# Performance work log

Measured on AMD Instinct MI355X. Metric: run time of the kernel, lower is better.

Reference implementation:

```python
import jax, jax.numpy as jnp
import numpy as np
from jax import lax

N, C_IN, H, W = 32, 128, 64, 64
C_OUT, KH, KW = 256, 3, 3
C_DIM = 64


def setup_inputs() -> dict:
    key = jax.random.key(0)
    k1, k2, k3, k4, k5 = jax.random.split(key, 5)
    return {
        "x": jax.random.normal(k1, (N, C_IN, H, W), dtype=jnp.float32),
        "c": jax.random.normal(k2, (N, C_DIM), dtype=jnp.float32),
        "weight": jax.random.normal(k3, (C_OUT, C_IN, KH, KW), dtype=jnp.float32),
        "c_weight": jax.random.normal(k4, (C_OUT, C_DIM), dtype=jnp.float32),
        "bias": jax.random.normal(k5, (C_OUT,), dtype=jnp.float32),
    }


def reference(x, c, weight, c_weight, bias):
    # Equivalent to the module's unfold + matmul path (groups=1, dilation=1,
    # zero padding=1, stride=1): a direct conv fused with the spatially
    # invariant context bias c @ c_weight^T and the channel bias.
    out = lax.conv_general_dilated(
        x, weight,
        window_strides=(1, 1),
        padding=((1, 1), (1, 1)),
        dimension_numbers=("NCHW", "OIHW", "NCHW"),
    )  # (N, C_out, H, W)
    ctx = jnp.einsum("nd,od->no", c, c_weight)  # (N, C_out), same at every spatial loc
    return out + ctx[:, :, None, None] + bias[None, :, None, None]
```

## Files before the change

kernel.cpp:

```cpp
#include <hip/hip_runtime.h>
#include <hip/hip_bf16.h>


#define NN   32
#define CIN  128
#define HH   64
#define WW   64
#define COUT 256
#define CDIM 64
#define HP   66
#define WP   66

#define XP_BYTES  ((size_t)NN*HP*WP*CIN*2)
#define WT_BYTES  ((size_t)9*COUT*CIN*2)
#define CTX_BYTES ((size_t)NN*COUT*4)
#define WS_NEEDED (XP_BYTES + WT_BYTES + CTX_BYTES)

typedef __attribute__((ext_vector_type(8))) short short8;
typedef __attribute__((ext_vector_type(4))) float float4v;

__device__ __forceinline__ void async16(const void* g, void* l) {
    __builtin_amdgcn_global_load_lds(
        (const __attribute__((address_space(1))) unsigned int*)g,
        (__attribute__((address_space(3))) unsigned int*)l, 16, 0, 0);
}

__global__ __launch_bounds__(256) void zero_halo(__hip_bfloat16* __restrict__ xP) {
    int g = blockIdx.x * 256 + threadIdx.x;
    int n   = g / 4160;
    int rem = g - n * 4160;
    int pi  = rem >> 4;
    int oct = rem & 15;
    int hh, ww;
    if (pi < 132) { hh = (pi >= 66) ? 65 : 0; ww = pi % 66; }
    else { int p2 = pi - 132; ww = (p2 >= 64) ? 65 : 0; hh = 1 + (p2 & 63); }
    short8 z = {};
    *(short8*)(xP + (((size_t)n * HP + hh) * WP + ww) * CIN + oct * 8) = z;
}

__global__ __launch_bounds__(256) void prep_x(const float* __restrict__ x,
                                              __hip_bfloat16* __restrict__ xP) {
    __shared__ float tile[CIN][65];
    int n = blockIdx.x >> 6;
    int h = blockIdx.x & 63;
    int t = threadIdx.x;
    const float* xb = x + (size_t)n * CIN * HH * WW + (size_t)h * WW;

    int lane16 = t & 15, rgrp = t >> 4;
    #pragma unroll
    for (int i = 0; i < 8; ++i) {
        int ci = rgrp + i * 16;
        float4v v = *(const float4v*)(xb + (size_t)ci * (HH * WW) + lane16 * 4);
        int w0 = lane16 * 4;
        tile[ci][w0]     = v.x;
        tile[ci][w0 + 1] = v.y;
        tile[ci][w0 + 2] = v.z;
        tile[ci][w0 + 3] = v.w;
    }
    __syncthreads();

    int oct = t & 3, w = t >> 2;
    __hip_bfloat16* db = xP + (((size_t)n * HP + (h + 1)) * WP + (w + 1)) * CIN;
    #pragma unroll
    for (int p = 0; p < 4; ++p) {
        int ci0 = p * 32 + oct * 8;
        union { short8 v; __hip_bfloat16 b[8]; } u;
        #pragma unroll
        for (int j = 0; j < 8; ++j)
            u.b[j] = __float2bfloat16(tile[ci0 + j][w]);
        *(short8*)(db + ci0) = u.v;
    }
}

__global__ __launch_bounds__(256) void prep_wc(const float* __restrict__ wgt,
                                               const float* __restrict__ c,
                                               const float* __restrict__ cw,
                                               const float* __restrict__ bias,
                                               __hip_bfloat16* __restrict__ wT,
                                               float* __restrict__ ctx) {
    int bid = blockIdx.x;
    if (bid < 1152) {
        int idx = bid * 256 + threadIdx.x;
        int ci  = idx & 127;
        int co  = (idx >> 7) & 255;
        int tap = idx >> 15;
        wT[idx] = __float2bfloat16(wgt[((size_t)co * CIN + ci) * 9 + tap]);
    } else {
        int idx = (bid - 1152) * 256 + threadIdx.x;
        int co = idx & 255, n = idx >> 8;
        float a = bias[co];
        #pragma unroll 8
        for (int d = 0; d < CDIM; ++d) a += c[n * CDIM + d] * cw[co * CDIM + d];
        ctx[idx] = a;
    }
}

__global__ __launch_bounds__(256) void conv_mfma(
    const __hip_bfloat16* __restrict__ xP,
    const __hip_bfloat16* __restrict__ wT,
    const float* __restrict__ ctx,
    float* __restrict__ out)
{
    __shared__ __align__(16) short A_s[8192];
    __shared__ __align__(16) short B_s[8192];

    int bid = blockIdx.x;
    int nt  = bid & 1;
    int mt  = bid >> 1;
    int n   = mt >> 5;
    int h0  = (mt & 31) << 1;

    int tid = threadIdx.x;
    int lane = tid & 63, wv = tid >> 6;
    int m0 = (wv & 1) * 64, n0 = (wv >> 1) * 64;

    int p0   = wv * 8 + (lane >> 3);
    int q8   = ((lane & 7) ^ (lane >> 3)) * 8;
    int dst0 = wv * 512 + lane * 8;

    int cofs0 = ((0 * 4 + (lane >> 4)) ^ (lane & 7)) * 8;
    int cofs1 = ((1 * 4 + (lane >> 4)) ^ (lane & 7)) * 8;

    float4v acc[4][4] = {};

    for (int kh = 0; kh < 3; ++kh)
    for (int kw = 0; kw < 3; ++kw) {
        int tap = kh * 3 + kw;
        #pragma unroll
        for (int kb = 0; kb < 2; ++kb) {
            __syncthreads();
            #pragma unroll
            for (int i = 0; i < 4; ++i) {
                int p  = p0 + i * 32;
                int hh = h0 + (p >> 6) + kh;
                int ww = (p & 63) + kw;
                const __hip_bfloat16* asrc =
                    xP + (((size_t)n * HP + hh) * WP + ww) * CIN + kb * 64 + q8;
                async16(asrc, &A_s[i * 2048 + dst0]);
                const __hip_bfloat16* bsrc =
                    wT + ((size_t)tap * COUT + nt * 128 + p) * CIN + kb * 64 + q8;
                async16(bsrc, &B_s[i * 2048 + dst0]);
            }
            __syncthreads();

            #pragma unroll
            for (int kk = 0; kk < 2; ++kk) {
                int cofs = kk ? cofs1 : cofs0;
                short8 aF[4], bF[4];
                #pragma unroll
                for (int mi = 0; mi < 4; ++mi)
                    aF[mi] = *(const short8*)&A_s[(m0 + mi * 16 + (lane & 15)) * 64 + cofs];
                #pragma unroll
                for (int ni = 0; ni < 4; ++ni)
                    bF[ni] = *(const short8*)&B_s[(n0 + ni * 16 + (lane & 15)) * 64 + cofs];
                #pragma unroll
                for (int mi = 0; mi < 4; ++mi)
                    #pragma unroll
                    for (int ni = 0; ni < 4; ++ni)
                        acc[mi][ni] = __builtin_amdgcn_mfma_f32_16x16x32_bf16(
                            aF[mi], bF[ni], acc[mi][ni], 0, 0, 0);
            }
        }
    }

    #pragma unroll
    for (int ni = 0; ni < 4; ++ni) {
        int co = nt * 128 + n0 + ni * 16 + (lane & 15);
        float cv = ctx[n * COUT + co];
        #pragma unroll
        for (int mi = 0; mi < 4; ++mi) {
            int rp = m0 + mi * 16 + (lane >> 4) * 4;
            int hh = h0 + (rp >> 6);
            int ww = rp & 63;
            float4v v = acc[mi][ni] + cv;
            *(float4v*)&out[(((size_t)n * COUT + co) * HH + hh) * WW + ww] = v;
        }
    }
}

__global__ __launch_bounds__(256) void contextual_conv_f32(
    const float* __restrict__ x, const float* __restrict__ c,
    const float* __restrict__ wgt, const float* __restrict__ cw,
    const float* __restrict__ bias, float* __restrict__ out)
{
    int idx = blockIdx.x * 256 + threadIdx.x;
    int w = idx & 63, h = (idx >> 6) & 63, cb = (idx >> 12) & 63, n = idx >> 18;
    float acc[4];
    #pragma unroll
    for (int j = 0; j < 4; ++j) acc[j] = bias[cb + j * 64];
    const float* cp = c + n * CDIM;
    for (int d = 0; d < CDIM; ++d) {
        float cv = cp[d];
        #pragma unroll
        for (int j = 0; j < 4; ++j) acc[j] += cv * cw[(cb + j * 64) * CDIM + d];
    }
    const float* xn = x + (size_t)n * (CIN * HH * WW);
    for (int ci = 0; ci < CIN; ++ci) {
        const float* xc = xn + ci * (HH * WW);
        float wv[4][9];
        #pragma unroll
        for (int j = 0; j < 4; ++j) {
            const float* wp = wgt + ((cb + j * 64) * CIN + ci) * 9;
            #pragma unroll
            for (int k = 0; k < 9; ++k) wv[j][k] = wp[k];
        }
        #pragma unroll
        for (int kh = 0; kh < 3; ++kh) {
            int hh = h + kh - 1;
            if (hh < 0 || hh >= HH) continue;
            const float* xr = xc + hh * WW;
            #pragma unroll
            for (int kw = 0; kw < 3; ++kw) {
                int ww = w + kw - 1;
                if (ww < 0 || ww >= WW) continue;
                float xv = xr[ww];
                #pragma unroll
                for (int j = 0; j < 4; ++j) acc[j] += xv * wv[j][kh * 3 + kw];
            }
        }
    }
    size_t obase = (size_t)n * (COUT * HH * WW) + (size_t)h * WW + w;
    #pragma unroll
    for (int j = 0; j < 4; ++j)
        out[obase + (size_t)(cb + j * 64) * (HH * WW)] = acc[j];
}

extern "C" void kernel_launch(void* const* d_in, const int* in_sizes, int n_in,
                              void* d_out, int out_size, void* d_ws, size_t ws_size,
                              hipStream_t stream) {
    const float* x    = (const float*)d_in[0];
    const float* c    = (const float*)d_in[1];
    const float* wgt  = (const float*)d_in[2];
    const float* cw   = (const float*)d_in[3];
    const float* bias = (const float*)d_in[4];
    float* out = (float*)d_out;

    if (ws_size < WS_NEEDED) {
        const int total_threads = NN * 64 * HH * WW;
        contextual_conv_f32<<<total_threads / 256, 256, 0, stream>>>(x, c, wgt, cw, bias, out);
        return;
    }

    char* ws = (char*)d_ws;
    __hip_bfloat16* xP = (__hip_bfloat16*)ws;
    __hip_bfloat16* wT = (__hip_bfloat16*)(ws + XP_BYTES);
    float*          cx = (float*)(ws + XP_BYTES + WT_BYTES);

    zero_halo<<<520, 256, 0, stream>>>(xP);
    prep_x  <<<NN * HH, 256, 0, stream>>>(x, xP);
    prep_wc <<<1184, 256, 0, stream>>>(wgt, c, cw, bias, wT, cx);
    conv_mfma<<<2048, 256, 0, stream>>>(xP, wT, cx, out);
}
```

Measured before the change: 270.5 us.

## Merge prep kernels and enlarge conv tile with double-buffered LDS pipeline

Folds the halo-zeroing, input-transpose and weight/context prep kernels into one launch, cutting launch overhead. The conv kernel now uses 512-thread blocks computing 256 output pixels by all 256 output channels. That halves the weight reloads per pixel and doubles per-wave accumulator tiles (8x4). LDS is double-buffered so the next tap's async global-to-LDS loads overlap the current MFMA work, with one barrier per step. Block indices are swizzled across images. The costs are higher register and LDS use (128 KB), which lowers occupancy, and a grid of only 512 blocks.

```diff
diff --git a/kernel.cpp b/kernel.cpp
--- a/kernel.cpp
+++ b/kernel.cpp
@@ -25,155 +25,168 @@
         (__attribute__((address_space(3))) unsigned int*)l, 16, 0, 0);
 }
 
-__global__ __launch_bounds__(256) void zero_halo(__hip_bfloat16* __restrict__ xP) {
-    int g = blockIdx.x * 256 + threadIdx.x;
-    int n   = g / 4160;
-    int rem = g - n * 4160;
-    int pi  = rem >> 4;
-    int oct = rem & 15;
-    int hh, ww;
-    if (pi < 132) { hh = (pi >= 66) ? 65 : 0; ww = pi % 66; }
-    else { int p2 = pi - 132; ww = (p2 >= 64) ? 65 : 0; hh = 1 + (p2 & 63); }
-    short8 z = {};
-    *(short8*)(xP + (((size_t)n * HP + hh) * WP + ww) * CIN + oct * 8) = z;
-}
-
-__global__ __launch_bounds__(256) void prep_x(const float* __restrict__ x,
-                                              __hip_bfloat16* __restrict__ xP) {
+__global__ __launch_bounds__(256) void prep_all(
+    const float* __restrict__ x, const float* __restrict__ c,
+    const float* __restrict__ wgt, const float* __restrict__ cw,
+    const float* __restrict__ bias,
+    __hip_bfloat16* __restrict__ xP, __hip_bfloat16* __restrict__ wT,
+    float* __restrict__ ctx)
+{
     __shared__ float tile[CIN][65];
-    int n = blockIdx.x >> 6;
-    int h = blockIdx.x & 63;
-    int t = threadIdx.x;
-    const float* xb = x + (size_t)n * CIN * HH * WW + (size_t)h * WW;
-
-    int lane16 = t & 15, rgrp = t >> 4;
-    #pragma unroll
-    for (int i = 0; i < 8; ++i) {
-        int ci = rgrp + i * 16;
-        float4v v = *(const float4v*)(xb + (size_t)ci * (HH * WW) + lane16 * 4);
-        int w0 = lane16 * 4;
-        tile[ci][w0]     = v.x;
-        tile[ci][w0 + 1] = v.y;
-        tile[ci][w0 + 2] = v.z;
-        tile[ci][w0 + 3] = v.w;
-    }
-    __syncthreads();
-
-    int oct = t & 3, w = t >> 2;
-    __hip_bfloat16* db = xP + (((size_t)n * HP + (h + 1)) * WP + (w + 1)) * CIN;
-    #pragma unroll
-    for (int p = 0; p < 4; ++p) {
-        int ci0 = p * 32 + oct * 8;
-        union { short8 v; __hip_bfloat16 b[8]; } u;
-        #pragma unroll
-        for (int j = 0; j < 8; ++j)
-            u.b[j] = __float2bfloat16(tile[ci0 + j][w]);
-        *(short8*)(db + ci0) = u.v;
-    }
-}
-
-__global__ __launch_bounds__(256) void prep_wc(const float* __restrict__ wgt,
-                                               const float* __restrict__ c,
-                                               const float* __restrict__ cw,
-                                               const float* __restrict__ bias,
-                                               __hip_bfloat16* __restrict__ wT,
-                                               float* __restrict__ ctx) {
     int bid = blockIdx.x;
-    if (bid < 1152) {
-        int idx = bid * 256 + threadIdx.x;
-        int ci  = idx & 127;
-        int co  = (idx >> 7) & 255;
-        int tap = idx >> 15;
-        wT[idx] = __float2bfloat16(wgt[((size_t)co * CIN + ci) * 9 + tap]);
+    int t   = threadIdx.x;
+
+    if (bid < 2048) {
+        int n = bid >> 6;
+        int h = bid & 63;
+        const float* xb = x + (size_t)n * CIN * HH * WW + (size_t)h * WW;
+
+        int lane16 = t & 15, rgrp = t >> 4;
+        #pragma unroll
+        for (int i = 0; i < 8; ++i) {
+            int ci = rgrp + i * 16;
+            float4v v = *(const float4v*)(xb + (size_t)ci * (HH * WW) + lane16 * 4);
+            int w0 = lane16 * 4;
+            tile[ci][w0]     = v.x;
+            tile[ci][w0 + 1] = v.y;
+            tile[ci][w0 + 2] = v.z;
+            tile[ci][w0 + 3] = v.w;
+        }
+        __syncthreads();
+
+        int oct = t & 3, w = t >> 2;
+        __hip_bfloat16* db = xP + (((size_t)n * HP + (h + 1)) * WP + (w + 1)) * CIN;
+        #pragma unroll
+        for (int p = 0; p < 4; ++p) {
+            int ci0 = p * 32 + oct * 8;
+            union { short8 v; __hip_bfloat16 b[8]; } u;
+            #pragma unroll
+            for (int j = 0; j < 8; ++j)
+                u.b[j] = __float2bfloat16(tile[ci0 + j][w]);
+            *(short8*)(db + ci0) = u.v;
+        }
+    } else if (bid < 2568) {
+        int g = (bid - 2048) * 256 + t;
+        int n   = g / 4160;
+        int rem = g - n * 4160;
+        int pi  = rem >> 4;
+        int oct = rem & 15;
+        int hh, ww;
+        if (pi < 132) { hh = (pi >= 66) ? 65 : 0; ww = pi % 66; }
+        else { int p2 = pi - 132; ww = (p2 >= 64) ? 65 : 0; hh = 1 + (p2 & 63); }
+        short8 z = {};
+        *(short8*)(xP + (((size_t)n * HP + hh) * WP + ww) * CIN + oct * 8) = z;
     } else {
-        int idx = (bid - 1152) * 256 + threadIdx.x;
-        int co = idx & 255, n = idx >> 8;
-        float a = bias[co];
-        #pragma unroll 8
-        for (int d = 0; d < CDIM; ++d) a += c[n * CDIM + d] * cw[co * CDIM + d];
-        ctx[idx] = a;
-    }
-}
-
-__global__ __launch_bounds__(256) void conv_mfma(
+        int b2 = bid - 2568;
+        if (b2 < 1152) {
+            int idx = b2 * 256 + t;
+            int ci  = idx & 127;
+            int co  = (idx >> 7) & 255;
+            int tap = idx >> 15;
+            wT[idx] = __float2bfloat16(wgt[((size_t)co * CIN + ci) * 9 + tap]);
+        } else {
+            int idx = (b2 - 1152) * 256 + t;
+            int co = idx & 255, n = idx >> 8;
+            float a = bias[co];
+            #pragma unroll 8
+            for (int d = 0; d < CDIM; ++d) a += c[n * CDIM + d] * cw[co * CDIM + d];
+            ctx[idx] = a;
+        }
+    }
+}
+
+__global__ __launch_bounds__(512) void conv_mfma(
     const __hip_bfloat16* __restrict__ xP,
     const __hip_bfloat16* __restrict__ wT,
     const float* __restrict__ ctx,
     float* __restrict__ out)
 {
-    __shared__ __align__(16) short A_s[8192];
-    __shared__ __align__(16) short B_s[8192];
+    __shared__ __align__(16) short A_s[2][16384];
+    __shared__ __align__(16) short B_s[2][16384];
 
     int bid = blockIdx.x;
-    int nt  = bid & 1;
-    int mt  = bid >> 1;
-    int n   = mt >> 5;
-    int h0  = (mt & 31) << 1;
-
-    int tid = threadIdx.x;
+    int mt  = (bid & 7) * 64 + (bid >> 3);
+    int n   = mt >> 4;
+    int h0  = (mt & 15) << 2;
+
+    int tid  = threadIdx.x;
     int lane = tid & 63, wv = tid >> 6;
-    int m0 = (wv & 1) * 64, n0 = (wv >> 1) * 64;
-
-    int p0   = wv * 8 + (lane >> 3);
-    int q8   = ((lane & 7) ^ (lane >> 3)) * 8;
-    int dst0 = wv * 512 + lane * 8;
-
-    int cofs0 = ((0 * 4 + (lane >> 4)) ^ (lane & 7)) * 8;
-    int cofs1 = ((1 * 4 + (lane >> 4)) ^ (lane & 7)) * 8;
-
-    float4v acc[4][4] = {};
-
-    for (int kh = 0; kh < 3; ++kh)
-    for (int kw = 0; kw < 3; ++kw) {
-        int tap = kh * 3 + kw;
-        #pragma unroll
-        for (int kb = 0; kb < 2; ++kb) {
-            __syncthreads();
+    int wm = (wv & 1) * 128;
+    int wn = (wv >> 1) * 64;
+
+    int rr  = tid >> 3;
+    int q8  = ((tid & 7) ^ (rr & 7)) << 3;
+    int stg = tid * 8;
+    const __hip_bfloat16* xA = xP + ((size_t)(n * HP + h0) * WP + rr) * CIN + q8;
+    const __hip_bfloat16* xB = wT + (size_t)rr * CIN + q8;
+
+    int l15   = lane & 15;
+    int rowA  = (wm + l15) << 6;
+    int rowB  = (wn + l15) << 6;
+    int cofs0 = (((lane >> 4)    ) ^ (lane & 7)) << 3;
+    int cofs1 = (((lane >> 4) + 4) ^ (lane & 7)) << 3;
+
+    float4v acc[8][4] = {};
+
+    #pragma unroll
+    for (int i = 0; i < 4; ++i) {
+        async16(xA + i * (WP * CIN), &A_s[0][i * 4096 + stg]);
+        async16(xB + i * (64 * CIN), &B_s[0][i * 4096 + stg]);
+    }
+
+    for (int s = 0; s < 18; ++s) {
+        int cur = s & 1;
+        __syncthreads();
+
+        if (s < 17) {
+            int s1  = s + 1;
+            int tap = s1 >> 1, kb = s1 & 1;
+            int kh  = (tap * 11) >> 5;
+            int kw  = tap - kh * 3;
+            const __hip_bfloat16* a1 = xA + (kh * WP + kw) * CIN + kb * 64;
+            const __hip_bfloat16* b1 = xB + tap * (COUT * CIN) + kb * 64;
+            short* Ad = A_s[cur ^ 1];
+            short* Bd = B_s[cur ^ 1];
             #pragma unroll
             for (int i = 0; i < 4; ++i) {
-                int p  = p0 + i * 32;
-                int hh = h0 + (p >> 6) + kh;
-                int ww = (p & 63) + kw;
-                const __hip_bfloat16* asrc =
-                    xP + (((size_t)n * HP + hh) * WP + ww) * CIN + kb * 64 + q8;
-                async16(asrc, &A_s[i * 2048 + dst0]);
-                const __hip_bfloat16* bsrc =
-                    wT + ((size_t)tap * COUT + nt * 128 + p) * CIN + kb * 64 + q8;
-                async16(bsrc, &B_s[i * 2048 + dst0]);
+                async16(a1 + i * (WP * CIN), Ad + i * 4096 + stg);
+                async16(b1 + i * (64 * CIN), Bd + i * 4096 + stg);
             }
-            __syncthreads();
-
-            #pragma unroll
-            for (int kk = 0; kk < 2; ++kk) {
-                int cofs = kk ? cofs1 : cofs0;
-                short8 aF[4], bF[4];
-                #pragma unroll
-                for (int mi = 0; mi < 4; ++mi)
-                    aF[mi] = *(const short8*)&A_s[(m0 + mi * 16 + (lane & 15)) * 64 + cofs];
+        }
+
+        const short* Ab = A_s[cur];
+        const short* Bb = B_s[cur];
+        #pragma unroll
+        for (int kk = 0; kk < 2; ++kk) {
+            int cofs = kk ? cofs1 : cofs0;
+            short8 aF[8], bF[4];
+            #pragma unroll
+            for (int mi = 0; mi < 8; ++mi)
+                aF[mi] = *(const short8*)&Ab[rowA + mi * 1024 + cofs];
+            #pragma unroll
+            for (int ni = 0; ni < 4; ++ni)
+                bF[ni] = *(const short8*)&Bb[rowB + ni * 1024 + cofs];
+            #pragma unroll
+            for (int mi = 0; mi < 8; ++mi)
                 #pragma unroll
                 for (int ni = 0; ni < 4; ++ni)
-                    bF[ni] = *(const short8*)&B_s[(n0 + ni * 16 + (lane & 15)) * 64 + cofs];
-                #pragma unroll
-                for (int mi = 0; mi < 4; ++mi)
-                    #pragma unroll
-                    for (int ni = 0; ni < 4; ++ni)
-                        acc[mi][ni] = __builtin_amdgcn_mfma_f32_16x16x32_bf16(
-                            aF[mi], bF[ni], acc[mi][ni], 0, 0, 0);
-            }
+                    acc[mi][ni] = __builtin_amdgcn_mfma_f32_16x16x32_bf16(
+                        aF[mi], bF[ni], acc[mi][ni], 0, 0, 0);
         }
     }
 
     #pragma unroll
     for (int ni = 0; ni < 4; ++ni) {
-        int co = nt * 128 + n0 + ni * 16 + (lane & 15);
+        int co = wn + ni * 16 + l15;
         float cv = ctx[n * COUT + co];
-        #pragma unroll
-        for (int mi = 0; mi < 4; ++mi) {
-            int rp = m0 + mi * 16 + (lane >> 4) * 4;
+        float* ob = out + ((size_t)n * COUT + co) * (HH * WW);
+        #pragma unroll
+        for (int mi = 0; mi < 8; ++mi) {
+            int rp = wm + mi * 16 + ((lane >> 4) << 2);
             int hh = h0 + (rp >> 6);
             int ww = rp & 63;
             float4v v = acc[mi][ni] + cv;
-            *(float4v*)&out[(((size_t)n * COUT + co) * HH + hh) * WW + ww] = v;
+            *(float4v*)&ob[hh * WW + ww] = v;
         }
     }
 }
@@ -246,8 +259,6 @@
     __hip_bfloat16* wT = (__hip_bfloat16*)(ws + XP_BYTES);
     float*          cx = (float*)(ws + XP_BYTES + WT_BYTES);
 
-    zero_halo<<<520, 256, 0, stream>>>(xP);
-    prep_x  <<<NN * HH, 256, 0, stream>>>(x, xP);
-    prep_wc <<<1184, 256, 0, stream>>>(wgt, c, cw, bias, wT, cx);
-    conv_mfma<<<2048, 256, 0, stream>>>(xP, wT, cx, out);
-}
+    prep_all <<<3752, 256, 0, stream>>>(x, c, wgt, cw, bias, xP, wT, cx);
+    conv_mfma<<<512, 512, 0, stream>>>(xP, wT, cx, out);
+}
```

New measurement: 268.2 us. About the same (-0.9%).
